# Performance work log

Measured on AMD Instinct MI355X. Metric: run time of the kernel, lower is better.

Reference implementation:

```python
import jax, jax.numpy as jnp
import numpy as np

DIM = 512
HEADS = 8
DIM_HEAD = 64
HIDDEN = HEADS * DIM_HEAD  # 512
SCALE = DIM_HEAD ** -0.5
EPS = 1e-12  # F.normalize default eps


def rms_norm(x, g):
    # F.normalize over channel dim (dim=1), then * g * sqrt(C)
    c = x.shape[1]
    norm = jnp.sqrt(jnp.sum(x * x, axis=1, keepdims=True))
    return x / jnp.maximum(norm, EPS) * g * (c ** 0.5)


def setup_inputs() -> dict:
    key = jax.random.key(0)
    ks = jax.random.split(key, 6)
    b, h, w = 16, 64, 64
    x = jax.random.normal(ks[0], (b, DIM, h, w), dtype=jnp.float32)
    g1 = jnp.ones((1, DIM, 1, 1), dtype=jnp.float32)
    # 1x1 conv weights stored as (out_ch, in_ch)
    Wqkv = jax.random.normal(ks[1], (HIDDEN * 3, DIM), dtype=jnp.float32) * (DIM ** -0.5)
    Wout = jax.random.normal(ks[2], (DIM, HIDDEN), dtype=jnp.float32) * (HIDDEN ** -0.5)
    bout = jax.random.normal(ks[3], (DIM,), dtype=jnp.float32) * 0.01
    g2 = jnp.ones((1, DIM, 1, 1), dtype=jnp.float32)
    return {"x": x, "g1": g1, "Wqkv": Wqkv, "Wout": Wout, "bout": bout, "g2": g2}


def reference(x, g1, Wqkv, Wout, bout, g2):
    b, c, h, w = x.shape
    n = h * w
    xn = rms_norm(x, g1)
    # 1x1 conv == channel matmul
    qkv = jnp.einsum('oc,bchw->bohw', Wqkv, xn)  # (b, 3*hidden, h, w)
    qkv = qkv.reshape(b, 3, HEADS, DIM_HEAD, n)
    q, k, v = qkv[:, 0], qkv[:, 1], qkv[:, 2]  # (b, heads, d, n)
    q = jax.nn.softmax(q, axis=-2) * SCALE      # softmax over feature dim
    k = jax.nn.softmax(k, axis=-1)               # softmax over spatial dim
    context = jnp.einsum('bhdn,bhen->bhde', k, v)  # (b,h,d,e) small
    out = jnp.einsum('bhde,bhdn->bhen', context, q)  # (b,h,e,n)
    out = out.reshape(b, HIDDEN, h, w)
    out = jnp.einsum('oc,bchw->bohw', Wout, out) + bout[None, :, None, None]
    return rms_norm(out, g2)
```

## Files before the change

### kernel.cpp

```cpp
#include <hip/hip_runtime.h>
#include <hip/hip_bf16.h>
#include <math.h>

#define B_ 16
#define C_ 512
#define N_ 4096
#define NCOL (B_ * N_)

typedef short bf16x8 __attribute__((ext_vector_type(8)));
typedef ushort ushort8_t __attribute__((ext_vector_type(8)));
typedef float f32x4 __attribute__((ext_vector_type(4)));

__device__ __forceinline__ ushort f2bf(float f) {
    unsigned u = __float_as_uint(f);
    unsigned r = (u + 0x7FFFu + ((u >> 16) & 1u)) >> 16;
    return (ushort)r;
}
__device__ __forceinline__ float bf2f(ushort u) {
    return __uint_as_float((unsigned)u << 16);
}
__device__ __forceinline__ void gload_lds16(const void* g, void* l) {
    __builtin_amdgcn_global_load_lds(
        (const __attribute__((address_space(1))) unsigned int*)g,
        (__attribute__((address_space(3))) unsigned int*)l, 16, 0, 0);
}

__global__ __launch_bounds__(256) void wprep_k(const float* __restrict__ W,
                                               const float* __restrict__ g,
                                               ushort* __restrict__ Wb, int nvec)
{
    int i = blockIdx.x * 256 + threadIdx.x;
    if (i >= nvec) return;
    float4 wv = reinterpret_cast<const float4*>(W)[i];
    if (g) {
        const float4 gv = *reinterpret_cast<const float4*>(g + ((i * 4) & 511));
        wv.x *= gv.x; wv.y *= gv.y; wv.z *= gv.z; wv.w *= gv.w;
    }
    ushort4 u;
    u.x = f2bf(wv.x); u.y = f2bf(wv.y); u.z = f2bf(wv.z); u.w = f2bf(wv.w);
    reinterpret_cast<ushort4*>(Wb)[i] = u;
}

__global__ __launch_bounds__(256) void transpose_k(const float* __restrict__ X,
                                                   ushort* __restrict__ Xt,
                                                   float* __restrict__ csq1)
{
    __shared__ float t[64][65];
    __shared__ float sq[4][64];
    const int b = blockIdx.z, n0 = blockIdx.x * 64, c0 = blockIdx.y * 64;
    const int tid = threadIdx.x;
    const int tx = tid & 63, ty = tid >> 6;
    const float* xp = X + ((size_t)b * C_ + c0) * N_ + n0;
    float local = 0.f;
    #pragma unroll
    for (int i = 0; i < 16; ++i) {
        float v = xp[(size_t)(ty + 4 * i) * N_ + tx];
        t[ty + 4 * i][tx] = v;
        local += v * v;
    }
    sq[ty][tx] = local;
    __syncthreads();
    #pragma unroll
    for (int i = 0; i < 4; ++i) {
        int nl = (tid >> 4) + i * 16;
        int cl = (tid & 15) * 4;
        ushort4 u;
        u.x = f2bf(t[cl + 0][nl]);
        u.y = f2bf(t[cl + 1][nl]);
        u.z = f2bf(t[cl + 2][nl]);
        u.w = f2bf(t[cl + 3][nl]);
        *reinterpret_cast<ushort4*>(Xt + ((size_t)b * N_ + n0 + nl) * 512 + c0 + cl) = u;
    }
    if (tid < 64)
        csq1[(size_t)blockIdx.y * NCOL + (size_t)b * N_ + n0 + tid] =
            sq[0][tid] + sq[1][tid] + sq[2][tid] + sq[3][tid];
}

__global__ __launch_bounds__(256) void rs1_reduce_k(const float* __restrict__ csq1,
                                                    float* __restrict__ rs1)
{
    int col = blockIdx.x * 256 + threadIdx.x;
    float s = 0.f;
    #pragma unroll
    for (int j = 0; j < 8; ++j) s += csq1[(size_t)j * NCOL + col];
    rs1[col] = 22.627416998f / fmaxf(sqrtf(s), 1e-12f);
}

__global__ __launch_bounds__(512, 2)
void mfma_gemm(const ushort* __restrict__ A, const ushort* __restrict__ Bt,
               const float* __restrict__ rs1,
               ushort* __restrict__ qT2, ushort* __restrict__ kd,
               ushort* __restrict__ vd)
{
    __shared__ __align__(16) char lds[2][2][32768];
    const int b  = blockIdx.z;
    const int n0 = blockIdx.x * 256;
    const int m0 = blockIdx.y * 256;
    const int tid = threadIdx.x;
    const int w = tid >> 6, l = tid & 63;
    const int wm = w >> 2, wn = w & 3;
    const int lq = l >> 4, lr = l & 15;
    const ushort* Bb = Bt + (size_t)b * N_ * 512;

    f32x4 acc[8][4];
    #pragma unroll
    for (int i = 0; i < 8; ++i)
        #pragma unroll
        for (int j = 0; j < 4; ++j)
            #pragma unroll
            for (int r = 0; r < 4; ++r) acc[i][j][r] = 0.f;

#define STAGE_STEP(t, i)                                                      \
    do {                                                                      \
        const int kb_ = (t) * 128;                                            \
        const int idx_ = (i) * 512 + tid;                                     \
        const int r_ = idx_ >> 3;                                             \
        const int ch_ = (idx_ & 7) ^ (r_ & 7);                                \
        gload_lds16((const char*)A + (size_t)(m0 + r_) * 1024 + kb_ + ch_ * 16,\
                    &lds[(t) & 1][0][idx_ * 16]);                             \
        gload_lds16((const char*)Bb + (size_t)(n0 + r_) * 1024 + kb_ + ch_ * 16,\
                    &lds[(t) & 1][1][idx_ * 16]);                             \
    } while (0)

    #pragma unroll
    for (int i = 0; i < 4; ++i) STAGE_STEP(0, i);

    bf16x8 bfr[4];
    #pragma unroll 2
    for (int t = 0; t < 8; ++t) {
        const char* As = lds[t & 1][0];
        const char* Bs = lds[t & 1][1];
        #pragma unroll
        for (int ph = 0; ph < 4; ++ph) {
            const int kk = ph >> 1, mg = ph & 1;
            bf16x8 af[4];
            if (ph != 0) {
                #pragma unroll
                for (int m2 = 0; m2 < 4; ++m2) {
                    int ra = wm * 128 + (mg * 4 + m2) * 16 + lr;
                    int ch = (kk * 4 + lq) ^ (ra & 7);
                    af[m2] = *(const bf16x8*)(As + ra * 128 + ch * 16);
                }
                if (mg == 0) {
                    #pragma unroll
                    for (int nf = 0; nf < 4; ++nf) {
                        int rb = wn * 64 + nf * 16 + lr;
                        int ch = (kk * 4 + lq) ^ (rb & 7);
                        bfr[nf] = *(const bf16x8*)(Bs + rb * 128 + ch * 16);
                    }
                }
            }
            if (t < 7) STAGE_STEP(t + 1, ph);
            if (ph == 0) {
                if (t < 7) { asm volatile("s_waitcnt vmcnt(2)" ::: "memory"); }
                else       { asm volatile("s_waitcnt vmcnt(0)" ::: "memory"); }
            }
            __builtin_amdgcn_s_barrier();
            if (ph == 0) {
                #pragma unroll
                for (int m2 = 0; m2 < 4; ++m2) {
                    int ra = wm * 128 + m2 * 16 + lr;
                    int ch = lq ^ (ra & 7);
                    af[m2] = *(const bf16x8*)(As + ra * 128 + ch * 16);
                }
                #pragma unroll
                for (int nf = 0; nf < 4; ++nf) {
                    int rb = wn * 64 + nf * 16 + lr;
                    int ch = lq ^ (rb & 7);
                    bfr[nf] = *(const bf16x8*)(Bs + rb * 128 + ch * 16);
                }
            }
            asm volatile("s_waitcnt lgkmcnt(0)" ::: "memory");
            __builtin_amdgcn_sched_barrier(0);
            __builtin_amdgcn_s_setprio(1);
            #pragma unroll
            for (int m2 = 0; m2 < 4; ++m2)
                #pragma unroll
                for (int nf = 0; nf < 4; ++nf)
                    acc[mg * 4 + m2][nf] = __builtin_amdgcn_mfma_f32_16x16x32_bf16(
                        af[m2], bfr[nf], acc[mg * 4 + m2][nf], 0, 0, 0);
            __builtin_amdgcn_s_setprio(0);
            __builtin_amdgcn_s_barrier();
        }
    }
#undef STAGE_STEP

    const int part = m0 >> 9;
    const int mloc = (m0 & 511) + wm * 128;
    const int nbase = n0 + wn * 64;
    if (part == 0) {
        #pragma unroll
        for (int hg = 0; hg < 2; ++hg) {
            const int head = (mloc >> 6) + hg;
            #pragma unroll
            for (int nf = 0; nf < 4; ++nf) {
                const int n = nbase + nf * 16 + lr;
                const float sc = rs1[(size_t)b * N_ + n];
                float v[4][4];
                float mx = -1e30f;
                #pragma unroll
                for (int m2 = 0; m2 < 4; ++m2)
                    #pragma unroll
                    for (int r = 0; r < 4; ++r) {
                        v[m2][r] = acc[hg * 4 + m2][nf][r] * sc;
                        mx = fmaxf(mx, v[m2][r]);
                    }
                mx = fmaxf(mx, __shfl_xor(mx, 16));
                mx = fmaxf(mx, __shfl_xor(mx, 32));
                float s = 0.f;
                #pragma unroll
                for (int m2 = 0; m2 < 4; ++m2)
                    #pragma unroll
                    for (int r = 0; r < 4; ++r) {
                        v[m2][r] = __expf(v[m2][r] - mx);
                        s += v[m2][r];
                    }
                s += __shfl_xor(s, 16);
                s += __shfl_xor(s, 32);
                const float r8 = 0.125f / s;
                ushort* qp = qT2 + ((size_t)b * N_ + n) * 512 + head * 64;
                #pragma unroll
                for (int m2 = 0; m2 < 4; ++m2) {
                    ushort4 u;
                    u.x = f2bf(v[m2][0] * r8);
                    u.y = f2bf(v[m2][1] * r8);
                    u.z = f2bf(v[m2][2] * r8);
                    u.w = f2bf(v[m2][3] * r8);
                    *reinterpret_cast<ushort4*>(qp + m2 * 16 + lq * 4) = u;
                }
            }
        }
    } else {
        ushort* dst = (part == 1) ? kd : vd;
        #pragma unroll
        for (int nf = 0; nf < 4; ++nf) {
            const int n = nbase + nf * 16 + lr;
            const float sc = rs1[(size_t)b * N_ + n];
            #pragma unroll
            for (int mf = 0; mf < 8; ++mf) {
                const int o = mloc + mf * 16 + lq * 4;
                #pragma unroll
                for (int r = 0; r < 4; ++r)
                    dst[((size_t)b * 512 + o + r) * N_ + n] =
                        f2bf(acc[mf][nf][r] * sc);
            }
        }
    }
}

__global__ __launch_bounds__(256) void rowstat_k(const ushort* __restrict__ kk,
                                                 float* __restrict__ rowm,
                                                 float* __restrict__ rowr)
{
    const int row = blockIdx.x * 4 + (threadIdx.x >> 6);
    const int lane = threadIdx.x & 63;
    const ushort* p = kk + (size_t)row * N_;
    float vals[64];
    #pragma unroll
    for (int j = 0; j < 8; ++j) {
        ushort8_t u = *reinterpret_cast<const ushort8_t*>(p + lane * 8 + j * 512);
        #pragma unroll
        for (int t = 0; t < 8; ++t) vals[j * 8 + t] = bf2f(u[t]);
    }
    float mx = -1e30f;
    #pragma unroll
    for (int i = 0; i < 64; ++i) mx = fmaxf(mx, vals[i]);
    #pragma unroll
    for (int o = 32; o >= 1; o >>= 1) mx = fmaxf(mx, __shfl_xor(mx, o));
    float s = 0.f;
    #pragma unroll
    for (int i = 0; i < 64; ++i) s += __expf(vals[i] - mx);
    #pragma unroll
    for (int o = 32; o >= 1; o >>= 1) s += __shfl_xor(s, o);
    if (lane == 0) { rowm[row] = mx; rowr[row] = 1.f / s; }
}

__global__ __launch_bounds__(256) void ctx_k(const ushort* __restrict__ kk,
                                             const ushort* __restrict__ vv,
                                             const float* __restrict__ rowm,
                                             const float* __restrict__ rowr,
                                             float* __restrict__ ctxp)
{
    const int bh = blockIdx.x, chunk = blockIdx.y;
    const ushort* kp = kk + (size_t)bh * 64 * N_;
    const ushort* vp = vv + (size_t)bh * 64 * N_;
    __shared__ __align__(16) ushort kx[64 * 128];
    __shared__ __align__(16) ushort vx[64 * 128];
    __shared__ float rm[64];
    const int tid = threadIdx.x;
    const int w = tid >> 6, l = tid & 63;
    const int lq = l >> 4, lr = l & 15;
    const int we = w >> 1, wd = w & 1;
    if (tid < 64) rm[tid] = rowm[(size_t)bh * 64 + tid];
    __syncthreads();

    f32x4 acc[2][2];
    #pragma unroll
    for (int i = 0; i < 2; ++i)
        #pragma unroll
        for (int j = 0; j < 2; ++j)
            #pragma unroll
            for (int r = 0; r < 4; ++r) acc[i][j][r] = 0.f;

    for (int s = 0; s < 8; ++s) {
        const int n0 = chunk * 1024 + s * 128;
        #pragma unroll
        for (int i = 0; i < 4; ++i) {
            int idx = i * 256 + tid;
            int row = idx >> 4;
            int ch  = (idx & 15) ^ (row & 15);
            gload_lds16((const char*)(vp + (size_t)row * N_ + n0 + ch * 8),
                        (char*)vx + idx * 16);
        }
        #pragma unroll
        for (int i = 0; i < 4; ++i) {
            int idx = i * 256 + tid;
            int row = idx >> 4;
            int ch  = idx & 15;
            ushort8_t u = *reinterpret_cast<const ushort8_t*>(
                kp + (size_t)row * N_ + n0 + ch * 8);
            float m_ = rm[row];
            ushort8_t o;
            #pragma unroll
            for (int t = 0; t < 8; ++t) o[t] = f2bf(__expf(bf2f(u[t]) - m_));
            *(ushort8_t*)((char*)kx + (row * 16 + (ch ^ (row & 15))) * 16) = o;
        }
        __syncthreads();
        #pragma unroll
        for (int k2 = 0; k2 < 4; ++k2) {
            bf16x8 af[2], bfr[2];
            #pragma unroll
            for (int i = 0; i < 2; ++i) {
                int re = we * 32 + i * 16 + lr;
                int cha = (k2 * 4 + lq) ^ (re & 15);
                af[i] = *(const bf16x8*)((const char*)vx + (re * 16 + cha) * 16);
                int rd = wd * 32 + i * 16 + lr;
                int chb = (k2 * 4 + lq) ^ (rd & 15);
                bfr[i] = *(const bf16x8*)((const char*)kx + (rd * 16 + chb) * 16);
            }
            #pragma unroll
            for (int i = 0; i < 2; ++i)
                #pragma unroll
                for (int j = 0; j < 2; ++j)
                    acc[i][j] = __builtin_amdgcn_mfma_f32_16x16x32_bf16(
                        af[i], bfr[j], acc[i][j], 0, 0, 0);
        }
        __syncthreads();
    }
    float* cbase = ctxp + ((size_t)bh * 4 + chunk) * 4096;
    #pragma unroll
    for (int j = 0; j < 2; ++j) {
        const int d = wd * 32 + j * 16 + lr;
        const float rr = rowr[(size_t)bh * 64 + d];
        #pragma unroll
        for (int i = 0; i < 2; ++i) {
            const int e0 = we * 32 + i * 16 + lq * 4;
            float4 wv;
            wv.x = acc[i][j][0] * rr;
            wv.y = acc[i][j][1] * rr;
            wv.z = acc[i][j][2] * rr;
            wv.w = acc[i][j][3] * rr;
            *reinterpret_cast<float4*>(cbase + (size_t)d * 64 + e0) = wv;
        }
    }
}

__global__ __launch_bounds__(256) void wcbuild_k(const ushort* __restrict__ Wb,
                                                 const float* __restrict__ ctxp,
                                                 ushort* __restrict__ Wc)
{
    const int oh = blockIdx.x, h = blockIdx.y, b = blockIdx.z;
    const int bh = b * 8 + h;
    __shared__ __align__(16) ushort ws[256 * 64];
    __shared__ __align__(16) ushort cs[64 * 64];
    const int tid = threadIdx.x;
    const int w = tid >> 6, l = tid & 63;
    const int lq = l >> 4, lr = l & 15;

    #pragma unroll
    for (int i = 0; i < 8; ++i) {
        int idx = i * 256 + tid;
        int row = idx >> 3;
        int ch = (idx & 7) ^ (row & 7);
        gload_lds16(Wb + (size_t)(oh * 256 + row) * 512 + h * 64 + ch * 8,
                    (char*)ws + idx * 16);
    }
    {
        const float* cp = ctxp + (size_t)bh * 4 * 4096;
        const int d = tid >> 2, eb = (tid & 3) * 16;
        float vs[16];
        #pragma unroll
        for (int t4 = 0; t4 < 4; ++t4) {
            float4 a0 = *(const float4*)(cp + d * 64 + eb + t4 * 4);
            float4 a1 = *(const float4*)(cp + 4096 + d * 64 + eb + t4 * 4);
            float4 a2 = *(const float4*)(cp + 8192 + d * 64 + eb + t4 * 4);
            float4 a3 = *(const float4*)(cp + 12288 + d * 64 + eb + t4 * 4);
            vs[t4 * 4 + 0] = a0.x + a1.x + a2.x + a3.x;
            vs[t4 * 4 + 1] = a0.y + a1.y + a2.y + a3.y;
            vs[t4 * 4 + 2] = a0.z + a1.z + a2.z + a3.z;
            vs[t4 * 4 + 3] = a0.w + a1.w + a2.w + a3.w;
        }
        ushort8_t o0, o1;
        #pragma unroll
        for (int t = 0; t < 8; ++t) { o0[t] = f2bf(vs[t]); o1[t] = f2bf(vs[8 + t]); }
        const int c0 = (eb >> 3) ^ (d & 7);
        const int c1 = ((eb >> 3) + 1) ^ (d & 7);
        *(ushort8_t*)((char*)cs + (d * 8 + c0) * 16) = o0;
        *(ushort8_t*)((char*)cs + (d * 8 + c1) * 16) = o1;
    }
    __syncthreads();

    f32x4 acc[4][4];
    #pragma unroll
    for (int i = 0; i < 4; ++i)
        #pragma unroll
        for (int j = 0; j < 4; ++j)
            #pragma unroll
            for (int r = 0; r < 4; ++r) acc[i][j][r] = 0.f;

    #pragma unroll
    for (int kk = 0; kk < 2; ++kk) {
        bf16x8 af[4], bfr[4];
        #pragma unroll
        for (int mf = 0; mf < 4; ++mf) {
            int ra = w * 64 + mf * 16 + lr;
            int ch = (kk * 4 + lq) ^ (ra & 7);
            af[mf] = *(const bf16x8*)((const char*)ws + (ra * 8 + ch) * 16);
        }
        #pragma unroll
        for (int nf = 0; nf < 4; ++nf) {
            int rd = nf * 16 + lr;
            int ch = (kk * 4 + lq) ^ (rd & 7);
            bfr[nf] = *(const bf16x8*)((const char*)cs + (rd * 8 + ch) * 16);
        }
        #pragma unroll
        for (int mf = 0; mf < 4; ++mf)
            #pragma unroll
            for (int nf = 0; nf < 4; ++nf)
                acc[mf][nf] = __builtin_amdgcn_mfma_f32_16x16x32_bf16(
                    af[mf], bfr[nf], acc[mf][nf], 0, 0, 0);
    }

    ushort* wp = Wc + (size_t)b * 262144 + h * 64;
    #pragma unroll
    for (int mf = 0; mf < 4; ++mf)
        #pragma unroll
        for (int r = 0; r < 4; ++r) {
            const int o = oh * 256 + w * 64 + mf * 16 + lq * 4 + r;
            #pragma unroll
            for (int nf = 0; nf < 4; ++nf)
                wp[(size_t)o * 512 + nf * 16 + lr] = f2bf(acc[mf][nf][r]);
        }
}

__global__ __launch_bounds__(512, 2)
void gemm2_k(const ushort* __restrict__ Wc,
             const ushort* __restrict__ Bt,
             const float* __restrict__ bias,
             const float* __restrict__ g2,
             float* __restrict__ outp)
{
    __shared__ __align__(16) ushort As[512 * 64];
    __shared__ __align__(16) ushort Bs[128 * 64];
    const int b  = blockIdx.y;
    const int n0 = blockIdx.x * 128;
    const int tid = threadIdx.x;
    const int w = tid >> 6, l = tid & 63;
    const int lq = l >> 4, lr = l & 15;
    const ushort* A  = Wc + (size_t)b * 262144;
    const ushort* Bb = Bt + (size_t)b * N_ * 512;

    f32x4 acc[4][8];
    #pragma unroll
    for (int i = 0; i < 4; ++i)
        #pragma unroll
        for (int j = 0; j < 8; ++j)
            #pragma unroll
            for (int r = 0; r < 4; ++r) acc[i][j][r] = 0.f;

    for (int k0 = 0; k0 < 512; k0 += 64) {
        #pragma unroll
        for (int i = 0; i < 8; ++i) {
            int base = i * 512 + w * 64;
            int idx = base + l;
            int r = idx >> 3, ch = (idx & 7) ^ (r & 7);
            gload_lds16((const char*)A + (size_t)r * 1024 + k0 * 2 + ch * 16,
                        (char*)As + (size_t)base * 16);
        }
        #pragma unroll
        for (int i = 0; i < 2; ++i) {
            int base = i * 512 + w * 64;
            int idx = base + l;
            int r = idx >> 3, ch = (idx & 7) ^ (r & 7);
            gload_lds16((const char*)Bb + (size_t)(n0 + r) * 1024 + k0 * 2 + ch * 16,
                        (char*)Bs + (size_t)base * 16);
        }
        __syncthreads();
        #pragma unroll
        for (int kk = 0; kk < 2; ++kk) {
            bf16x8 af[4], bfv[8];
            #pragma unroll
            for (int mf = 0; mf < 4; ++mf) {
                int ra = w * 64 + mf * 16 + lr;
                int ch = (kk * 4 + lq) ^ (ra & 7);
                af[mf] = *(const bf16x8*)((const char*)As + ra * 128 + ch * 16);
            }
            #pragma unroll
            for (int nf = 0; nf < 8; ++nf) {
                int rb = nf * 16 + lr;
                int ch = (kk * 4 + lq) ^ (rb & 7);
                bfv[nf] = *(const bf16x8*)((const char*)Bs + rb * 128 + ch * 16);
            }
            #pragma unroll
            for (int mf = 0; mf < 4; ++mf)
                #pragma unroll
                for (int nf = 0; nf < 8; ++nf)
                    acc[mf][nf] = __builtin_amdgcn_mfma_f32_16x16x32_bf16(
                        af[mf], bfv[nf], acc[mf][nf], 0, 0, 0);
        }
        __syncthreads();
    }

    float4 bv[4], g2v[4];
    #pragma unroll
    for (int mf = 0; mf < 4; ++mf) {
        bv[mf]  = *reinterpret_cast<const float4*>(bias + w * 64 + mf * 16 + lq * 4);
        g2v[mf] = *reinterpret_cast<const float4*>(g2   + w * 64 + mf * 16 + lq * 4);
    }
    float csq[8] = {};
    #pragma unroll
    for (int mf = 0; mf < 4; ++mf)
        #pragma unroll
        for (int nf = 0; nf < 8; ++nf)
            #pragma unroll
            for (int r = 0; r < 4; ++r) {
                float wv = acc[mf][nf][r] + ((const float*)&bv[mf])[r];
                acc[mf][nf][r] = wv;
                csq[nf] += wv * wv;
            }
    #pragma unroll
    for (int nf = 0; nf < 8; ++nf) {
        csq[nf] += __shfl_xor(csq[nf], 16);
        csq[nf] += __shfl_xor(csq[nf], 32);
    }
    float* red  = (float*)As;
    float* rs2s = red + 1024;
    if (lq == 0) {
        #pragma unroll
        for (int nf = 0; nf < 8; ++nf)
            red[w * 128 + nf * 16 + lr] = csq[nf];
    }
    __syncthreads();
    if (tid < 128) {
        float s = 0.f;
        #pragma unroll
        for (int j = 0; j < 8; ++j) s += red[j * 128 + tid];
        rs2s[tid] = 22.627416998f / fmaxf(sqrtf(s), 1e-12f);
    }
    __syncthreads();
    #pragma unroll
    for (int nf = 0; nf < 8; ++nf) {
        const float rsv = rs2s[nf * 16 + lr];
        const int n = n0 + nf * 16 + lr;
        #pragma unroll
        for (int mf = 0; mf < 4; ++mf) {
            const int o = w * 64 + mf * 16 + lq * 4;
            float* p = outp + ((size_t)b * 512 + o) * N_ + n;
            #pragma unroll
            for (int r = 0; r < 4; ++r)
                p[(size_t)r * N_] = acc[mf][nf][r] * rsv * ((const float*)&g2v[mf])[r];
        }
    }
}

extern "C" void kernel_launch(void* const* d_in, const int* in_sizes, int n_in,
                              void* d_out, int out_size, void* d_ws, size_t ws_size,
                              hipStream_t stream)
{
    const float* x    = (const float*)d_in[0];
    const float* g1   = (const float*)d_in[1];
    const float* Wqkv = (const float*)d_in[2];
    const float* Wout = (const float*)d_in[3];
    const float* bout = (const float*)d_in[4];
    const float* g2   = (const float*)d_in[5];
    float* out = (float*)d_out;

    char* wsb = (char*)d_ws;
    ushort* qbuf  = (ushort*)wsb;
    float*  csq1  = (float*)wsb;
    ushort* kbuf  = (ushort*)(wsb + ((size_t)64 << 20));
    ushort* vbuf  = (ushort*)(wsb + ((size_t)128 << 20));
    ushort* Xt    = (ushort*)(wsb + ((size_t)192 << 20));
    float*  ctxp  = (float*)Xt;
    float*  rowm  = (float*)(wsb + ((size_t)200 << 20));
    float*  rowr  = rowm + 8192;
    ushort* Wcb   = (ushort*)(wsb + ((size_t)201 << 20));
    char*   tail  = wsb + ((size_t)256 << 20);
    ushort* Wqkvb = (ushort*)tail;
    ushort* Woutb = (ushort*)(tail + (size_t)1536 * 512 * 2);
    float*  rs1   = (float*)(tail + (size_t)1536 * 512 * 2 + (size_t)512 * 512 * 2);

    wprep_k<<<768, 256, 0, stream>>>(Wqkv, g1, Wqkvb, 1536 * 512 / 4);
    wprep_k<<<256, 256, 0, stream>>>(Wout, nullptr, Woutb, 512 * 512 / 4);
    transpose_k<<<dim3(64, 8, 16), 256, 0, stream>>>(x, Xt, csq1);
    rs1_reduce_k<<<256, 256, 0, stream>>>(csq1, rs1);
    mfma_gemm<<<dim3(16, 6, B_), 512, 0, stream>>>(Wqkvb, Xt, rs1,
                                                   qbuf, kbuf, vbuf);
    rowstat_k<<<2048, 256, 0, stream>>>(kbuf, rowm, rowr);
    ctx_k<<<dim3(B_ * 8, 4), 256, 0, stream>>>(kbuf, vbuf, rowm, rowr, ctxp);
    wcbuild_k<<<dim3(2, 8, B_), 256, 0, stream>>>(Woutb, ctxp, Wcb);
    gemm2_k<<<dim3(32, B_), 512, 0, stream>>>(Wcb, qbuf, bout, g2, out);
}
```

Measured before the change: 300.8 us.

## Fuse norm reduction into transpose, merge weight prep, coalesce k/v stores via LDS

The two weight-prep launches become one, and the column sum-of-squares reduction moves into the transpose kernel. Each transpose block now loops over all 512 channels, so it can write rs1 directly and the csq1 buffer and its reduce kernel go away. The QKV GEMM is split into two template instantiations. For k/v the MFMA operands are swapped so the accumulator is transposed, and results are staged through swizzled LDS to emit 16-byte row-contiguous stores instead of scattered 2-byte writes. The trade is fewer transpose blocks, with lower parallelism and a serial chunk loop, plus an extra GEMM launch.

New measurement: 320.7 us. 1.07x slower.

```diff
diff --git a/kernel.cpp b/kernel.cpp
--- a/kernel.cpp
+++ b/kernel.cpp
@@ -25,77 +25,85 @@
         (__attribute__((address_space(3))) unsigned int*)l, 16, 0, 0);
 }
 
-__global__ __launch_bounds__(256) void wprep_k(const float* __restrict__ W,
-                                               const float* __restrict__ g,
-                                               ushort* __restrict__ Wb, int nvec)
+__global__ __launch_bounds__(256) void wprep2_k(const float* __restrict__ Wqkv,
+                                                const float* __restrict__ g1,
+                                                const float* __restrict__ Wout,
+                                                ushort* __restrict__ Wqkvb,
+                                                ushort* __restrict__ Woutb)
 {
     int i = blockIdx.x * 256 + threadIdx.x;
-    if (i >= nvec) return;
-    float4 wv = reinterpret_cast<const float4*>(W)[i];
-    if (g) {
-        const float4 gv = *reinterpret_cast<const float4*>(g + ((i * 4) & 511));
-        wv.x *= gv.x; wv.y *= gv.y; wv.z *= gv.z; wv.w *= gv.w;
-    }
-    ushort4 u;
-    u.x = f2bf(wv.x); u.y = f2bf(wv.y); u.z = f2bf(wv.z); u.w = f2bf(wv.w);
-    reinterpret_cast<ushort4*>(Wb)[i] = u;
+    if (i < 196608) {
+        float4 wv = reinterpret_cast<const float4*>(Wqkv)[i];
+        const float4 gv = *reinterpret_cast<const float4*>(g1 + ((i * 4) & 511));
+        ushort4 u;
+        u.x = f2bf(wv.x * gv.x); u.y = f2bf(wv.y * gv.y);
+        u.z = f2bf(wv.z * gv.z); u.w = f2bf(wv.w * gv.w);
+        reinterpret_cast<ushort4*>(Wqkvb)[i] = u;
+    } else {
+        int j = i - 196608;
+        float4 wv = reinterpret_cast<const float4*>(Wout)[j];
+        ushort4 u;
+        u.x = f2bf(wv.x); u.y = f2bf(wv.y); u.z = f2bf(wv.z); u.w = f2bf(wv.w);
+        reinterpret_cast<ushort4*>(Woutb)[j] = u;
+    }
 }
 
 __global__ __launch_bounds__(256) void transpose_k(const float* __restrict__ X,
                                                    ushort* __restrict__ Xt,
-                                                   float* __restrict__ csq1)
-{
-    __shared__ float t[64][65];
-    __shared__ float sq[4][64];
-    const int b = blockIdx.z, n0 = blockIdx.x * 64, c0 = blockIdx.y * 64;
+                                                   float* __restrict__ rs1)
+{
+    __shared__ float t[2][64][68];
+    __shared__ float sr[16][64];
+    const int b = blockIdx.y, n0 = blockIdx.x * 64;
     const int tid = threadIdx.x;
-    const int tx = tid & 63, ty = tid >> 6;
-    const float* xp = X + ((size_t)b * C_ + c0) * N_ + n0;
-    float local = 0.f;
-    #pragma unroll
-    for (int i = 0; i < 16; ++i) {
-        float v = xp[(size_t)(ty + 4 * i) * N_ + tx];
-        t[ty + 4 * i][tx] = v;
-        local += v * v;
-    }
-    sq[ty][tx] = local;
+    const int tg = tid >> 4, tl = tid & 15;
+    float sq[4] = {0.f, 0.f, 0.f, 0.f};
+    for (int chunk = 0; chunk < 8; ++chunk) {
+        const int buf = chunk & 1;
+        const float* xp = X + ((size_t)b * C_ + chunk * 64) * N_ + n0;
+        #pragma unroll
+        for (int j = 0; j < 4; ++j) {
+            int c = tg + j * 16;
+            float4 v = *reinterpret_cast<const float4*>(xp + (size_t)c * N_ + tl * 4);
+            *reinterpret_cast<float4*>(&t[buf][c][tl * 4]) = v;
+            sq[0] += v.x * v.x; sq[1] += v.y * v.y;
+            sq[2] += v.z * v.z; sq[3] += v.w * v.w;
+        }
+        __syncthreads();
+        #pragma unroll
+        for (int i = 0; i < 4; ++i) {
+            int nl = tg + i * 16, cl = tl * 4;
+            ushort4 u;
+            u.x = f2bf(t[buf][cl + 0][nl]);
+            u.y = f2bf(t[buf][cl + 1][nl]);
+            u.z = f2bf(t[buf][cl + 2][nl]);
+            u.w = f2bf(t[buf][cl + 3][nl]);
+            *reinterpret_cast<ushort4*>(
+                Xt + ((size_t)b * N_ + n0 + nl) * 512 + chunk * 64 + cl) = u;
+        }
+    }
+    #pragma unroll
+    for (int j = 0; j < 4; ++j) sr[tg][tl * 4 + j] = sq[j];
     __syncthreads();
-    #pragma unroll
-    for (int i = 0; i < 4; ++i) {
-        int nl = (tid >> 4) + i * 16;
-        int cl = (tid & 15) * 4;
-        ushort4 u;
-        u.x = f2bf(t[cl + 0][nl]);
-        u.y = f2bf(t[cl + 1][nl]);
-        u.z = f2bf(t[cl + 2][nl]);
-        u.w = f2bf(t[cl + 3][nl]);
-        *reinterpret_cast<ushort4*>(Xt + ((size_t)b * N_ + n0 + nl) * 512 + c0 + cl) = u;
-    }
-    if (tid < 64)
-        csq1[(size_t)blockIdx.y * NCOL + (size_t)b * N_ + n0 + tid] =
-            sq[0][tid] + sq[1][tid] + sq[2][tid] + sq[3][tid];
-}
-
-__global__ __launch_bounds__(256) void rs1_reduce_k(const float* __restrict__ csq1,
-                                                    float* __restrict__ rs1)
-{
-    int col = blockIdx.x * 256 + threadIdx.x;
-    float s = 0.f;
-    #pragma unroll
-    for (int j = 0; j < 8; ++j) s += csq1[(size_t)j * NCOL + col];
-    rs1[col] = 22.627416998f / fmaxf(sqrtf(s), 1e-12f);
-}
-
+    if (tid < 64) {
+        float s = 0.f;
+        #pragma unroll
+        for (int g = 0; g < 16; ++g) s += sr[g][tid];
+        rs1[(size_t)b * N_ + n0 + tid] = 22.627416998f / fmaxf(sqrtf(s), 1e-12f);
+    }
+}
+
+template <bool SWAP>
 __global__ __launch_bounds__(512, 2)
 void mfma_gemm(const ushort* __restrict__ A, const ushort* __restrict__ Bt,
                const float* __restrict__ rs1,
                ushort* __restrict__ qT2, ushort* __restrict__ kd,
-               ushort* __restrict__ vd)
+               ushort* __restrict__ vd, int m_off)
 {
     __shared__ __align__(16) char lds[2][2][32768];
     const int b  = blockIdx.z;
     const int n0 = blockIdx.x * 256;
-    const int m0 = blockIdx.y * 256;
+    const int m0 = m_off + blockIdx.y * 256;
     const int tid = threadIdx.x;
     const int w = tid >> 6, l = tid & 63;
     const int wm = w >> 2, wn = w & 3;
@@ -176,19 +184,23 @@
             #pragma unroll
             for (int m2 = 0; m2 < 4; ++m2)
                 #pragma unroll
-                for (int nf = 0; nf < 4; ++nf)
-                    acc[mg * 4 + m2][nf] = __builtin_amdgcn_mfma_f32_16x16x32_bf16(
-                        af[m2], bfr[nf], acc[mg * 4 + m2][nf], 0, 0, 0);
+                for (int nf = 0; nf < 4; ++nf) {
+                    if constexpr (SWAP)
+                        acc[mg * 4 + m2][nf] = __builtin_amdgcn_mfma_f32_16x16x32_bf16(
+                            bfr[nf], af[m2], acc[mg * 4 + m2][nf], 0, 0, 0);
+                    else
+                        acc[mg * 4 + m2][nf] = __builtin_amdgcn_mfma_f32_16x16x32_bf16(
+                            af[m2], bfr[nf], acc[mg * 4 + m2][nf], 0, 0, 0);
+                }
             __builtin_amdgcn_s_setprio(0);
             __builtin_amdgcn_s_barrier();
         }
     }
 #undef STAGE_STEP
 
-    const int part = m0 >> 9;
-    const int mloc = (m0 & 511) + wm * 128;
     const int nbase = n0 + wn * 64;
-    if (part == 0) {
+    if constexpr (!SWAP) {
+        const int mloc = (m0 & 511) + wm * 128;
         #pragma unroll
         for (int hg = 0; hg < 2; ++hg) {
             const int head = (mloc >> 6) + hg;
@@ -231,19 +243,36 @@
             }
         }
     } else {
+        const int part = m0 >> 9;
+        const int mloc = (m0 & 511) + wm * 128;
         ushort* dst = (part == 1) ? kd : vd;
-        #pragma unroll
-        for (int nf = 0; nf < 4; ++nf) {
-            const int n = nbase + nf * 16 + lr;
-            const float sc = rs1[(size_t)b * N_ + n];
-            #pragma unroll
-            for (int mf = 0; mf < 8; ++mf) {
-                const int o = mloc + mf * 16 + lq * 4;
-                #pragma unroll
-                for (int r = 0; r < 4; ++r)
-                    dst[((size_t)b * 512 + o + r) * N_ + n] =
-                        f2bf(acc[mf][nf][r] * sc);
-            }
+        float4 sc4[4];
+        #pragma unroll
+        for (int nf = 0; nf < 4; ++nf)
+            sc4[nf] = *reinterpret_cast<const float4*>(
+                rs1 + (size_t)b * N_ + nbase + nf * 16 + lq * 4);
+        #pragma unroll
+        for (int mf = 0; mf < 8; ++mf) {
+            char* reg = &lds[0][0][w * 4096 + (mf & 1) * 2048];
+            #pragma unroll
+            for (int nf = 0; nf < 4; ++nf) {
+                ushort4 u;
+                u.x = f2bf(acc[mf][nf][0] * sc4[nf].x);
+                u.y = f2bf(acc[mf][nf][1] * sc4[nf].y);
+                u.z = f2bf(acc[mf][nf][2] * sc4[nf].z);
+                u.w = f2bf(acc[mf][nf][3] * sc4[nf].w);
+                const int col2 = (nf * 16 + lq * 4) * 2;
+                *reinterpret_cast<ushort4*>(
+                    reg + lr * 128 + (col2 ^ ((lr & 7) << 4))) = u;
+            }
+            asm volatile("s_waitcnt lgkmcnt(0)" ::: "memory");
+            const int rho = l >> 3;
+            const int nc = (l & 7) * 16;
+            bf16x8 v0 = *(const bf16x8*)(reg + rho * 128 + (nc ^ ((rho & 7) << 4)));
+            bf16x8 v1 = *(const bf16x8*)(reg + (rho + 8) * 128 + (nc ^ ((rho & 7) << 4)));
+            const size_t ro = (size_t)b * 512 + mloc + mf * 16;
+            *(bf16x8*)(dst + (ro + rho) * N_ + nbase + (l & 7) * 8) = v0;
+            *(bf16x8*)(dst + (ro + rho + 8) * N_ + nbase + (l & 7) * 8) = v1;
         }
     }
 }
@@ -587,7 +616,6 @@
 
     char* wsb = (char*)d_ws;
     ushort* qbuf  = (ushort*)wsb;
-    float*  csq1  = (float*)wsb;
     ushort* kbuf  = (ushort*)(wsb + ((size_t)64 << 20));
     ushort* vbuf  = (ushort*)(wsb + ((size_t)128 << 20));
     ushort* Xt    = (ushort*)(wsb + ((size_t)192 << 20));
@@ -600,12 +628,12 @@
     ushort* Woutb = (ushort*)(tail + (size_t)1536 * 512 * 2);
     float*  rs1   = (float*)(tail + (size_t)1536 * 512 * 2 + (size_t)512 * 512 * 2);
 
-    wprep_k<<<768, 256, 0, stream>>>(Wqkv, g1, Wqkvb, 1536 * 512 / 4);
-    wprep_k<<<256, 256, 0, stream>>>(Wout, nullptr, Woutb, 512 * 512 / 4);
-    transpose_k<<<dim3(64, 8, 16), 256, 0, stream>>>(x, Xt, csq1);
-    rs1_reduce_k<<<256, 256, 0, stream>>>(csq1, rs1);
-    mfma_gemm<<<dim3(16, 6, B_), 512, 0, stream>>>(Wqkvb, Xt, rs1,
-                                                   qbuf, kbuf, vbuf);
+    wprep2_k<<<1024, 256, 0, stream>>>(Wqkv, g1, Wout, Wqkvb, Woutb);
+    transpose_k<<<dim3(64, 16), 256, 0, stream>>>(x, Xt, rs1);
+    mfma_gemm<false><<<dim3(16, 2, B_), 512, 0, stream>>>(Wqkvb, Xt, rs1,
+                                                          qbuf, kbuf, vbuf, 0);
+    mfma_gemm<true><<<dim3(16, 4, B_), 512, 0, stream>>>(Wqkvb, Xt, rs1,
+                                                         qbuf, kbuf, vbuf, 512);
     rowstat_k<<<2048, 256, 0, stream>>>(kbuf, rowm, rowr);
     ctx_k<<<dim3(B_ * 8, 4), 256, 0, stream>>>(kbuf, vbuf, rowm, rowr, ctxp);
     wcbuild_k<<<dim3(2, 8, B_), 256, 0, stream>>>(Woutb, ctxp, Wcb);
```
